# Performance work log

Hardware: AMD Instinct MI355X
Metric: run time of the kernel (lower is better)

## Reference

```python
import jax, jax.numpy as jnp
import numpy as np

# Model hyperparameters (match init_kwargs)
T = 3          # reasoning hops
L = 3          # rule channels (parallel LSTMs)
E = 50000      # number of entities
N = 1000000    # number of KG triples
R = 200        # r_size = (n-1)//2
NREL = 2 * R + 1  # n = 401 (forward rels, inverse rels, identity)
H = 256        # emb_size
TAU = 10.0     # tau_1 softmax temperature
TOPK = 1000    # top-k state pruning for hops t>=1
B = 8          # batch size


def setup_inputs() -> dict:
    key = jax.random.key(0)
    ks = jax.random.split(key, 16)
    s = 0.05
    return {
        "input_x": jax.random.randint(ks[0], (B,), 0, E),
        "input_r": jax.random.randint(ks[1], (B,), 0, NREL),
        "e2triple": jax.random.randint(ks[2], (3, N), 0, E),
        "triple2e": jax.random.randint(ks[3], (2, N), 0, E),
        "r2triple": jax.random.randint(ks[4], (1, N), 0, R),
        "emb": jax.random.normal(ks[5], (NREL, H), jnp.float32) * s,
        "Wih_f": jax.random.normal(ks[6], (L, 4 * H, H), jnp.float32) * s,
        "Whh_f": jax.random.normal(ks[7], (L, 4 * H, H), jnp.float32) * s,
        "bih_f": jax.random.normal(ks[8], (L, 4 * H), jnp.float32) * s,
        "bhh_f": jax.random.normal(ks[9], (L, 4 * H), jnp.float32) * s,
        "Wih_b": jax.random.normal(ks[10], (L, 4 * H, H), jnp.float32) * s,
        "Whh_b": jax.random.normal(ks[11], (L, 4 * H, H), jnp.float32) * s,
        "bih_b": jax.random.normal(ks[12], (L, 4 * H), jnp.float32) * s,
        "bhh_b": jax.random.normal(ks[13], (L, 4 * H), jnp.float32) * s,
        "linW": jax.random.normal(ks[14], (NREL, 2 * H), jnp.float32) * s,
        "linb": jax.random.normal(ks[15], (NREL,), jnp.float32) * s,
    }


def _lstm_scan(x, Wih, Whh, bih, bhh):
    # x: [S, B, H]; PyTorch gate order i, f, g, o. Returns hidden seq [S, B, H].
    Bn = x.shape[1]
    Hh = Whh.shape[1]
    pre = x @ Wih.T + bih + bhh  # hoist input projection out of the scan

    def step(carry, xt):
        h, c = carry
        g = xt + h @ Whh.T
        i, f, gg, o = jnp.split(g, 4, axis=-1)
        c = jax.nn.sigmoid(f) * c + jax.nn.sigmoid(i) * jnp.tanh(gg)
        h = jax.nn.sigmoid(o) * jnp.tanh(c)
        return (h, c), h

    init = (jnp.zeros((Bn, Hh), x.dtype), jnp.zeros((Bn, Hh), x.dtype))
    _, hs = jax.lax.scan(step, init, pre)
    return hs


def reference(input_x, input_r, e2triple, triple2e, r2triple, emb,
              Wih_f, Whh_f, bih_f, bhh_f, Wih_b, Whh_b, bih_b, bhh_b,
              linW, linb):
    Bsz = input_x.shape[0]
    x0 = jax.nn.one_hot(input_x, E, dtype=emb.dtype)  # [B, E] one-hot query entity
    q = emb[input_r]                                   # [B, H] query relation emb
    # [T+1, B, H]: T copies of the query rel emb, last step is the special emb[-1]
    seq = jnp.concatenate([
        jnp.broadcast_to(q[None], (T, Bsz, H)),
        jnp.broadcast_to(emb[-1][None, None, :], (1, Bsz, H)),
    ], axis=0)

    outs = []
    for l in range(L):  # small fixed number of structurally distinct LSTMs
        hf = _lstm_scan(seq, Wih_f[l], Whh_f[l], bih_f[l], bhh_f[l])
        hb = _lstm_scan(seq[::-1], Wih_b[l], Whh_b[l], bih_b[l], bhh_b[l])[::-1]
        rnn = jnp.concatenate([hf, hb], axis=-1).transpose(1, 0, 2)  # [B, T+1, 2H]
        outs.append(rnn[:, :-1] @ linW.T + linb)                      # [B, T, n]
    w_all = jnp.stack(outs, axis=2)  # [B, T, L, n]

    heads = e2triple[0]   # [N] head entity per triple
    tails = triple2e[1]   # [N] tail entity per triple
    tails2 = e2triple[2]  # [N] tail entity per triple (inverse-direction gather)
    rels = r2triple[0]    # [N] relation per triple, in [0, R)

    def propagate(x, w):
        # x: [B, *, E] entity state, w: [B, L, n] relation weights
        s_i = w[:, :, -1:] * x                              # identity relation
        msg_f = x[:, :, heads] * w[:, :, rels]              # [B, L, N] fwd messages
        s_h = jnp.zeros((Bsz, L, E), x.dtype).at[:, :, tails].add(msg_f)
        msg_b = x[:, :, tails2] * w[:, :, rels + R]         # inverse relations
        s_t = jnp.zeros((Bsz, L, E), x.dtype).at[:, :, heads].add(msg_b)
        return s_i + s_h + s_t

    def prune_topk(x, k):
        # keep top-k entity scores per (batch, channel), zero the rest
        th = jax.lax.top_k(x, k)[0][..., -1:]
        return jnp.where(x >= th, x, jnp.zeros((), x.dtype))

    s = None
    for t in range(T):
        w = jax.nn.softmax(w_all[:, t] / TAU, axis=-1)      # [B, L, n]
        xin = x0[:, None, :] if t == 0 else prune_topk(s, TOPK)
        st = propagate(xin, w)
        s = st / jnp.maximum(st.sum(-1, keepdims=True), 1e-7)
    return s.sum(axis=1)  # [B, E]
```

## Files before the change

### kernel.cpp

```cpp
#include <hip/hip_runtime.h>
#include <math.h>

#define TT 3
#define LL 3
#define EE 50000
#define NN 1000000
#define RR 200
#define NRELC 401
#define HH 256
#define BB 8
#define KTOP 1000
#define SROW 24
#define NBUCK 782
#define BSH 6
#define CSRN (2 * NN)
#define STB 512
#define SEGS 50176

__device__ __forceinline__ float sigmoidf_(float x) {
    if (x >= 0.f) { return 1.f / (1.f + expf(-x)); }
    float z = expf(x); return z / (1.f + z);
}

__global__ __launch_bounds__(256) void pre_fused(
    const int* __restrict__ input_r, const float* __restrict__ emb,
    const float* __restrict__ Wih_f, const float* __restrict__ bih_f, const float* __restrict__ bhh_f,
    const float* __restrict__ Wih_b, const float* __restrict__ bih_b, const float* __restrict__ bhh_b,
    float* __restrict__ preq, float* __restrict__ pree,
    float* __restrict__ hstate, float* __restrict__ cstate, float* __restrict__ hbuf2,
    const int* __restrict__ heads, const int* __restrict__ tails,
    unsigned* __restrict__ bh, int do_hist)
{
    if (blockIdx.x >= 384) {
        if (!do_hist) return;
        __shared__ unsigned h[NBUCK];
        int tid = threadIdx.x;
        int bid = blockIdx.x - 384;
        for (int i = tid; i < NBUCK; i += 256) h[i] = 0u;
        __syncthreads();
        for (int i = bid * 256 + tid; i < NN; i += STB * 256) {
            atomicAdd(&h[tails[i] >> BSH], 1u);
            atomicAdd(&h[heads[i] >> BSH], 1u);
        }
        __syncthreads();
        for (int j = tid; j < NBUCK; j += 256)
            bh[(size_t)j * STB + bid] = h[j];
        return;
    }
    int wave = blockIdx.x * 4 + (threadIdx.x >> 6);
    int lane = threadIdx.x & 63;
    int ld = wave >> 8;
    int j  = wave & 255;
    int l = ld >> 1, dir = ld & 1;
    const float* Wih = (dir ? Wih_b : Wih_f) + (size_t)l * 4 * HH * HH;
    const float* bih = (dir ? bih_b : bih_f) + l * 4 * HH;
    const float* bhh = (dir ? bhh_b : bhh_f) + l * 4 * HH;

    float4 xf[9];
    for (int b = 0; b < 8; ++b) {
        int r = input_r[b];
        xf[b] = *(const float4*)(emb + (size_t)r * HH + lane * 4);
    }
    xf[8] = *(const float4*)(emb + (size_t)(NRELC - 1) * HH + lane * 4);

    float g4[4], ge4[4];
    for (int q = 0; q < 4; ++q) {
        int row = q * 256 + j;
        float4 w4 = *(const float4*)(Wih + (size_t)row * HH + lane * 4);
        float acc[9];
        #pragma unroll
        for (int c = 0; c < 9; ++c)
            acc[c] = w4.x * xf[c].x + w4.y * xf[c].y + w4.z * xf[c].z + w4.w * xf[c].w;
        #pragma unroll
        for (int off = 32; off > 0; off >>= 1)
            #pragma unroll
            for (int c = 0; c < 9; ++c) acc[c] += __shfl_xor(acc[c], off);
        float bsum = bih[row] + bhh[row];
        g4[q]  = (lane < 8 ? acc[lane] : 0.f) + bsum;
        ge4[q] = acc[8] + bsum;
        if (lane < 8) preq[((size_t)ld * 8 + lane) * 1024 + row] = g4[q];
        if (lane == 8) pree[(size_t)ld * 1024 + row] = ge4[q];
    }
    if (lane < 8) {
        float gi, gg, go;
        if (dir == 0) { gi = g4[0]; gg = g4[2]; go = g4[3]; }
        else          { gi = ge4[0]; gg = ge4[2]; go = ge4[3]; }
        float c = sigmoidf_(gi) * tanhf(gg);
        float h = sigmoidf_(go) * tanhf(c);
        int g = (ld * 8 + lane) * 256 + j;
        cstate[g] = c;
        hstate[g] = h;
        if (dir == 0) hbuf2[(((size_t)ld * 8 + lane) * 3 + 0) * HH + j] = h;
    }
}

__global__ __launch_bounds__(256) void rec_fused(
    const float* __restrict__ Whh_f, const float* __restrict__ Whh_b,
    const float* __restrict__ preq, const float* __restrict__ pree,
    const float* __restrict__ hprev, float* __restrict__ hnext,
    float* __restrict__ cstate, float* __restrict__ hbuf2, int step)
{
    int wave = blockIdx.x * 4 + (threadIdx.x >> 6);
    int lane = threadIdx.x & 63;
    int ld = wave >> 8, j = wave & 255;
    int l = ld >> 1, dir = ld & 1;
    const float* Whh = (dir ? Whh_b : Whh_f) + (size_t)l * 4 * HH * HH;
    bool use_e = (dir == 0) && (step == 3);

    float4 hf[8];
    for (int b = 0; b < 8; ++b)
        hf[b] = *(const float4*)(hprev + ((size_t)ld * 8 + b) * HH + lane * 4);

    float g4[4];
    for (int q = 0; q < 4; ++q) {
        int row = q * 256 + j;
        float4 w4 = *(const float4*)(Whh + (size_t)row * HH + lane * 4);
        float acc[8];
        #pragma unroll
        for (int b = 0; b < 8; ++b)
            acc[b] = w4.x * hf[b].x + w4.y * hf[b].y + w4.z * hf[b].z + w4.w * hf[b].w;
        #pragma unroll
        for (int off = 32; off > 0; off >>= 1)
            #pragma unroll
            for (int b = 0; b < 8; ++b) acc[b] += __shfl_xor(acc[b], off);
        if (lane < 8) {
            float pre = use_e ? pree[(size_t)ld * 1024 + row]
                              : preq[((size_t)ld * 8 + lane) * 1024 + row];
            g4[q] = acc[lane] + pre;
        }
    }
    if (lane < 8) {
        int g = (ld * 8 + lane) * 256 + j;
        float c = cstate[g];
        float iv = sigmoidf_(g4[0]), fv = sigmoidf_(g4[1]);
        float gg = tanhf(g4[2]),     ov = sigmoidf_(g4[3]);
        c = fv * c + iv * gg;
        float h = ov * tanhf(c);
        cstate[g] = c;
        hnext[g] = h;
        int t_out = dir ? (3 - step) : step;
        if (t_out <= 2) hbuf2[(((size_t)ld * 8 + lane) * 3 + t_out) * HH + j] = h;
    }
}

__global__ __launch_bounds__(256) void logits_dot(
    const float* __restrict__ hbuf2, const float* __restrict__ linW,
    const float* __restrict__ linb, float* __restrict__ wbuf)
{
    int wave = blockIdx.x * 4 + (threadIdx.x >> 6);
    if (wave >= 3 * 3 * NRELC) return;
    int lane = threadIdx.x & 63;
    int n = wave % NRELC;
    int tc = wave / NRELC;
    int t = tc / 3, chunk = tc % 3;
    const float4* wr = (const float4*)(linW + (size_t)n * 2 * HH + lane * 8);
    float4 w4a = wr[0], w4b = wr[1];
    float acc[8];
    #pragma unroll
    for (int i = 0; i < 8; ++i) {
        int combo = chunk * 8 + i;
        int b = combo / 3, l = combo % 3;
        int ldh = (lane < 32) ? (l * 2 + 0) : (l * 2 + 1);
        const float* hsrc = hbuf2 + (((size_t)ldh * 8 + b) * 3 + t) * HH + (lane & 31) * 8;
        float4 f0 = *(const float4*)hsrc;
        float4 f1 = *(const float4*)(hsrc + 4);
        acc[i] = w4a.x * f0.x + w4a.y * f0.y + w4a.z * f0.z + w4a.w * f0.w
               + w4b.x * f1.x + w4b.y * f1.y + w4b.z * f1.z + w4b.w * f1.w;
    }
    #pragma unroll
    for (int off = 32; off > 0; off >>= 1)
        #pragma unroll
        for (int i = 0; i < 8; ++i) acc[i] += __shfl_xor(acc[i], off);
    if (lane < 8) {
        int combo = chunk * 8 + lane;
        wbuf[((size_t)t * 24 + combo) * NRELC + n] = acc[lane] + linb[n];
    }
}

__global__ __launch_bounds__(256) void softmax_kernel(float* __restrict__ wbuf) {
    int rowi = blockIdx.x;
    float* w = wbuf + (size_t)rowi * NRELC;
    __shared__ float red[256];
    int tid = threadIdx.x;
    float v0 = w[tid];
    float v1 = (tid + 256 < NRELC) ? w[tid + 256] : -1e30f;
    red[tid] = fmaxf(v0, v1); __syncthreads();
    for (int s2 = 128; s2 > 0; s2 >>= 1) {
        if (tid < s2) red[tid] = fmaxf(red[tid], red[tid + s2]);
        __syncthreads();
    }
    float m = red[0]; __syncthreads();
    float e0 = expf((v0 - m) * 0.1f);
    float e1 = (tid + 256 < NRELC) ? expf((v1 - m) * 0.1f) : 0.f;
    red[tid] = e0 + e1; __syncthreads();
    for (int s2 = 128; s2 > 0; s2 >>= 1) {
        if (tid < s2) red[tid] += red[tid + s2];
        __syncthreads();
    }
    float denom = red[0];
    w[tid] = e0 / denom;
    if (tid + 256 < NRELC) w[tid + 256] = e1 / denom;
}

__global__ __launch_bounds__(256) void fill_seed(
    float* __restrict__ s, const int* __restrict__ input_x, const float* __restrict__ w0,
    unsigned* __restrict__ rowcnt)
{
    __shared__ int xs[8];
    __shared__ float wv[24];
    if (threadIdx.x < 8) xs[threadIdx.x] = input_x[threadIdx.x];
    if (threadIdx.x < 24) wv[threadIdx.x] = w0[(size_t)threadIdx.x * NRELC + (NRELC - 1)];
    if (blockIdx.x == 0 && threadIdx.x < 24) rowcnt[threadIdx.x] = 0u;
    __syncthreads();
    int i = blockIdx.x * 256 + threadIdx.x;
    if (i >= SROW * EE) return;
    int row = i % 24;
    int e = i / 24;
    s[i] = (e == xs[row / 3]) ? wv[row] : 0.f;
}

__global__ __launch_bounds__(256) void hop0_scan(
    const int* __restrict__ heads, const int* __restrict__ tails,
    const int* __restrict__ tails2, const int* __restrict__ rels,
    const int* __restrict__ input_x, const float* __restrict__ w0,
    float* __restrict__ s)
{
    __shared__ int xs[BB];
    if (threadIdx.x < BB) xs[threadIdx.x] = input_x[threadIdx.x];
    __syncthreads();
    int i = blockIdx.x * 256 + threadIdx.x;
    if (i >= NN) return;
    int h = heads[i], t2 = tails2[i];
    bool any = false;
    #pragma unroll
    for (int b = 0; b < BB; ++b) any = any || (h == xs[b]) || (t2 == xs[b]);
    if (!any) return;
    int tl = tails[i], rr = rels[i];
    for (int b = 0; b < BB; ++b) {
        if (h == xs[b])
            for (int l = 0; l < LL; ++l)
                atomicAdd(&s[(size_t)tl * SROW + b * 3 + l], w0[(b * 3 + l) * NRELC + rr]);
        if (t2 == xs[b])
            for (int l = 0; l < LL; ++l)
                atomicAdd(&s[(size_t)h * SROW + b * 3 + l], w0[(b * 3 + l) * NRELC + rr + RR]);
    }
}

__global__ __launch_bounds__(256) void rowsum_compact(
    const float* __restrict__ s, float* __restrict__ partial,
    unsigned* __restrict__ ckey, unsigned* __restrict__ rowcnt, int do_compact)
{
    __shared__ float acc[24];
    __shared__ unsigned lkey[24][168];
    __shared__ unsigned lcnt[24];
    __shared__ unsigned lbase[24];
    int tid = threadIdx.x;
    if (tid < 24) { acc[tid] = 0.f; lcnt[tid] = 0u; }
    __syncthreads();
    int gidx = blockIdx.x * 256 + tid;
    int row = gidx % 24;
    float a = 0.f;
    const int total = SROW * EE;
    for (int k = 0; k < 13; ++k) {
        long i = (long)gidx + (long)k * 98304;
        if (i < total) {
            float v = s[i];
            a += v;
            if (do_compact && __float_as_uint(v) != 0u) {
                unsigned slot = atomicAdd(&lcnt[row], 1u);
                slot = min(slot, 167u);
                lkey[row][slot] = __float_as_uint(v);
            }
        }
    }
    if (do_compact) {
        __syncthreads();
        if (tid < 24) {
            unsigned c = min(lcnt[tid], 168u);
            lcnt[tid] = c;
            lbase[tid] = min(atomicAdd(&rowcnt[tid], c), (unsigned)SEGS);
        }
        __syncthreads();
        int r = tid % 24;
        int nthr = (r < 16) ? 11 : 10;
        unsigned cnt = lcnt[r], base = lbase[r];
        if (base + cnt > (unsigned)SEGS) cnt = (unsigned)SEGS - base;
        for (unsigned j = (unsigned)(tid / 24); j < cnt; j += nthr)
            ckey[(size_t)r * SEGS + base + j] = lkey[r][j];
        __syncthreads();
    }
    atomicAdd(&acc[row], a);
    __syncthreads();
    if (tid < 24) partial[blockIdx.x * 24 + tid] = acc[tid];
}

__global__ __launch_bounds__(256) void rowsum_fin(
    const float* __restrict__ partial, float* __restrict__ sums,
    const float* __restrict__ w_t, float* __restrict__ wsc,
    float* __restrict__ wTg)
{
    int r = blockIdx.x;
    int tid = threadIdx.x;
    __shared__ float sa;
    if (tid == 0) {
        float a = 0.f;
        for (int j = 0; j < 384; ++j) a += partial[j * 24 + r];
        a = fmaxf(a, 1e-7f);
        sums[r] = a;
        sa = a;
    }
    __syncthreads();
    if (w_t != nullptr) {
        float a = sa;
        for (int i = tid; i < NRELC; i += 256) {
            float v = w_t[(size_t)r * NRELC + i] / a;
            wsc[(size_t)r * NRELC + i] = v;
            if (wTg != nullptr && i < 2 * RR) wTg[(size_t)i * SROW + r] = v;
        }
    }
}

__global__ __launch_bounds__(256) void rowsum_fin2(
    const float* __restrict__ partial2, float* __restrict__ sums,
    const float* __restrict__ w_t, float* __restrict__ wsc,
    float* __restrict__ wTg)
{
    int r = blockIdx.x;
    int tid = threadIdx.x;
    __shared__ float red[256];
    float a = 0.f;
    for (int g = tid; g < NBUCK; g += 256) a += partial2[(size_t)g * 24 + r];
    red[tid] = a; __syncthreads();
    for (int s2 = 128; s2 > 0; s2 >>= 1) {
        if (tid < s2) red[tid] += red[tid + s2];
        __syncthreads();
    }
    __shared__ float sa;
    if (tid == 0) { sa = fmaxf(red[0], 1e-7f); sums[r] = sa; }
    __syncthreads();
    if (w_t != nullptr) {
        float aa = sa;
        for (int i = tid; i < NRELC; i += 256) {
            float v = w_t[(size_t)r * NRELC + i] / aa;
            wsc[(size_t)r * NRELC + i] = v;
            if (wTg != nullptr && i < 2 * RR) wTg[(size_t)i * SROW + r] = v;
        }
    }
}

__global__ __launch_bounds__(512) void topk_select(
    const unsigned* __restrict__ ckey, const unsigned* __restrict__ rowcnt,
    float* __restrict__ th, int* __restrict__ mask)
{
    int row = blockIdx.x, tid = threadIdx.x;
    {
        int per = (EE + 23) / 24;
        int e0 = row * per, e1 = min(e0 + per, EE);
        for (int e = e0 + tid; e < e1; e += 512) mask[e] = 0;
    }
    const unsigned* keys = ckey + (size_t)row * SEGS;
    int n = min((int)rowcnt[row], SEGS);
    __shared__ unsigned hist[256];
    __shared__ int red[256];
    __shared__ int sh_bin, sh_rem;
    unsigned prefix = 0;
    int remk = KTOP;
    int iters = (n + 511) / 512;
    int lane = tid & 63;
    for (int round = 0; round < 4; ++round) {
        if (tid < 256) hist[tid] = 0u;
        __syncthreads();
        int shift = 24 - 8 * round;
        for (int it = 0; it < iters; ++it) {
            int i = it * 512 + tid;
            bool valid = (i < n);
            unsigned key = valid ? keys[i] : 0u;
            valid = valid && (round == 0 || (key >> (shift + 8)) == prefix);
            unsigned bin = valid ? ((key >> shift) & 255u) : 0u;
            unsigned long long peers = __ballot(valid);
            #pragma unroll
            for (int bit = 0; bit < 8; ++bit) {
                unsigned long long bm = __ballot(valid && ((bin >> bit) & 1u));
                peers &= ((bin >> bit) & 1u) ? bm : ~bm;
            }
            if (valid) {
                unsigned long long lower = peers & ((1ull << lane) - 1ull);
                if (lower == 0ull)
                    atomicAdd(&hist[bin], (unsigned)__popcll(peers));
            }
        }
        __syncthreads();
        if (tid < 256) red[tid] = (int)hist[tid];
        __syncthreads();
        for (int off = 1; off < 256; off <<= 1) {
            int v = 0;
            if (tid < 256 && tid + off < 256) v = red[tid + off];
            __syncthreads();
            if (tid < 256) red[tid] += v;
            __syncthreads();
        }
        if (tid == 0) { sh_bin = 0; sh_rem = remk; }
        __syncthreads();
        if (tid < 256) {
            int cnt = (int)hist[tid];
            int above = (tid == 255) ? 0 : red[tid + 1];
            if (above < remk && above + cnt >= remk) { sh_bin = tid; sh_rem = remk - above; }
        }
        __syncthreads();
        prefix = (prefix << 8) | (unsigned)sh_bin;
        remk = sh_rem;
        __syncthreads();
    }
    if (tid == 0) th[row] = __uint_as_float(prefix);
}

__global__ __launch_bounds__(256) void prune_flat(
    float* __restrict__ s, const float* __restrict__ th,
    const float* __restrict__ wsc, float* __restrict__ x, int* __restrict__ mask,
    unsigned* __restrict__ rowcnt, int write_s)
{
    __shared__ float ths[24], w4s[24];
    if (threadIdx.x < 24) {
        ths[threadIdx.x] = th[threadIdx.x];
        w4s[threadIdx.x] = wsc[threadIdx.x * NRELC + (NRELC - 1)];
    }
    if (blockIdx.x == 0 && threadIdx.x < 24) rowcnt[threadIdx.x] = 0u;
    __syncthreads();
    int i = blockIdx.x * 256 + threadIdx.x;
    if (i >= SROW * EE) return;
    int row = i % 24;
    int e = i / 24;
    float v = s[i];
    float xv = (v >= ths[row]) ? v : 0.f;
    x[i] = xv;
    if (write_s) s[i] = w4s[row] * xv;
    if (xv > 0.f) atomicOr(&mask[e], 1 << (row / 3));
}

__global__ __launch_bounds__(256) void hop_scan(
    const int* __restrict__ heads, const int* __restrict__ tails,
    const int* __restrict__ tails2, const int* __restrict__ rels,
    const int* __restrict__ mask, const float* __restrict__ x,
    const float* __restrict__ wsc, float* __restrict__ s)
{
    int gid = blockIdx.x * 256 + threadIdx.x;
    int i = gid >> 3;
    if (i >= NN) return;
    int b = gid & 7;
    int h = heads[i], t2 = tails2[i];
    int mh = mask[h], mt = mask[t2];
    bool ah = (mh >> b) & 1;
    bool at = (mt >> b) & 1;
    if (!(ah || at)) return;
    int tl = tails[i], rr = rels[i];
    int row = b * 3;
    if (ah) {
        float v0 = x[(size_t)h * SROW + row];
        float v1 = x[(size_t)h * SROW + row + 1];
        float v2 = x[(size_t)h * SROW + row + 2];
        if (v0 != 0.f) atomicAdd(&s[(size_t)tl * SROW + row],     v0 * wsc[(row)     * NRELC + rr]);
        if (v1 != 0.f) atomicAdd(&s[(size_t)tl * SROW + row + 1], v1 * wsc[(row + 1) * NRELC + rr]);
        if (v2 != 0.f) atomicAdd(&s[(size_t)tl * SROW + row + 2], v2 * wsc[(row + 2) * NRELC + rr]);
    }
    if (at) {
        float v0 = x[(size_t)t2 * SROW + row];
        float v1 = x[(size_t)t2 * SROW + row + 1];
        float v2 = x[(size_t)t2 * SROW + row + 2];
        if (v0 != 0.f) atomicAdd(&s[(size_t)h * SROW + row],     v0 * wsc[(row)     * NRELC + rr + RR]);
        if (v1 != 0.f) atomicAdd(&s[(size_t)h * SROW + row + 1], v1 * wsc[(row + 1) * NRELC + rr + RR]);
        if (v2 != 0.f) atomicAdd(&s[(size_t)h * SROW + row + 2], v2 * wsc[(row + 2) * NRELC + rr + RR]);
    }
}

__global__ __launch_bounds__(512) void csr_scanb(
    unsigned* __restrict__ bh, unsigned* __restrict__ gcnt)
{
    __shared__ unsigned sc[STB];
    int bk = blockIdx.x, tid = threadIdx.x;
    unsigned v = bh[(size_t)bk * STB + tid];
    sc[tid] = v; __syncthreads();
    #pragma unroll
    for (int o = 1; o < STB; o <<= 1) {
        unsigned u = (tid >= o) ? sc[tid - o] : 0u;
        __syncthreads();
        sc[tid] += u;
        __syncthreads();
    }
    bh[(size_t)bk * STB + tid] = sc[tid] - v;
    if (tid == STB - 1) gcnt[bk] = sc[tid];
}

__global__ __launch_bounds__(1024) void csr_scan2(
    const unsigned* __restrict__ gcnt, unsigned* __restrict__ gOff)
{
    __shared__ unsigned sc[1024];
    int tid = threadIdx.x;
    unsigned v = (tid < NBUCK) ? gcnt[tid] : 0u;
    sc[tid] = v; __syncthreads();
    #pragma unroll
    for (int o = 1; o < 1024; o <<= 1) {
        unsigned u = (tid >= o) ? sc[tid - o] : 0u;
        __syncthreads();
        sc[tid] += u;
        __syncthreads();
    }
    if (tid < NBUCK) gOff[tid] = sc[tid] - v;
    if (tid == NBUCK - 1) gOff[NBUCK] = sc[tid];
}

__global__ __launch_bounds__(256) void csr_stage2(
    const int* __restrict__ heads, const int* __restrict__ tails,
    const int* __restrict__ tails2, const int* __restrict__ rels,
    const unsigned* __restrict__ gOff, const unsigned* __restrict__ bh,
    unsigned* __restrict__ staging)
{
    __shared__ unsigned base[NBUCK];
    __shared__ unsigned cur[NBUCK];
    int tid = threadIdx.x;
    for (int j = tid; j < NBUCK; j += 256) {
        base[j] = gOff[j] + bh[(size_t)j * STB + blockIdx.x];
        cur[j] = 0u;
    }
    __syncthreads();
    for (int i = blockIdx.x * 256 + tid; i < NN; i += STB * 256) {
        unsigned rl = (unsigned)rels[i];
        int h = heads[i], d1 = tails[i], t2 = tails2[i];
        unsigned p1 = base[d1 >> BSH] + atomicAdd(&cur[d1 >> BSH], 1u);
        if (p1 < (unsigned)CSRN)
            staging[p1] = ((unsigned)(d1 & 63) << 26) | ((unsigned)h << 9) | rl;
        unsigned p2 = base[h >> BSH] + atomicAdd(&cur[h >> BSH], 1u);
        if (p2 < (unsigned)CSRN)
            staging[p2] = ((unsigned)(h & 63) << 26) | ((unsigned)t2 << 9) | (rl + RR);
    }
}

__global__ __launch_bounds__(256) void hop_bucket(
    const unsigned* __restrict__ gOff, const unsigned* __restrict__ staging,
    const int* __restrict__ mask, const float* __restrict__ x,
    const float* __restrict__ wT, const float* __restrict__ wsc,
    float* __restrict__ s, float* __restrict__ partial2,
    unsigned* __restrict__ ckey, unsigned* __restrict__ rowcnt, int do_compact)
{
    __shared__ float sl[64][24];
    __shared__ float w4s[24];
    __shared__ float acc24[24];
    __shared__ unsigned lcnt[24];
    __shared__ unsigned lbase[24];
    __shared__ unsigned lkey[24][64];
    int bk = blockIdx.x, tid = threadIdx.x;
    for (int i = tid; i < 64 * 24; i += 256) ((float*)sl)[i] = 0.f;
    if (tid < 24) {
        w4s[tid] = wsc[tid * NRELC + (NRELC - 1)];
        acc24[tid] = 0.f;
        lcnt[tid] = 0u;
    }
    __syncthreads();
    unsigned j0 = gOff[bk], j1 = gOff[bk + 1];
    for (unsigned j = j0 + tid; j < j1; j += 256) {
        unsigned p = staging[j];
        int src = (int)((p >> 9) & 0xFFFFu);
        int m = mask[src];
        if (!m) continue;
        int dl = (int)(p >> 26);
        int rel = (int)(p & 511u);
        const float* xs = x + (size_t)src * SROW;
        const float* wr = wT + (size_t)rel * SROW;
        while (m) {
            int b = __ffs(m) - 1; m &= m - 1;
            int r = b * 3;
            atomicAdd(&sl[dl][r],     xs[r]     * wr[r]);
            atomicAdd(&sl[dl][r + 1], xs[r + 1] * wr[r + 1]);
            atomicAdd(&sl[dl][r + 2], xs[r + 2] * wr[r + 2]);
        }
    }
    __syncthreads();
    int e0 = bk * 64;
    for (int idx = tid; idx < 64 * 24; idx += 256) {
        int el = idx / 24, row = idx % 24;
        int e = e0 + el;
        if (e >= EE) continue;
        float v = sl[el][row] + w4s[row] * x[(size_t)e * SROW + row];
        s[(size_t)e * SROW + row] = v;
        atomicAdd(&acc24[row], v);
        if (do_compact && __float_as_uint(v) != 0u) {
            unsigned slot = atomicAdd(&lcnt[row], 1u);
            slot = min(slot, 63u);
            lkey[row][slot] = __float_as_uint(v);
        }
    }
    __syncthreads();
    if (tid < 24) partial2[(size_t)bk * 24 + tid] = acc24[tid];
    if (do_compact) {
        if (tid < 24) {
            unsigned c = min(lcnt[tid], 64u);
            lcnt[tid] = c;
            lbase[tid] = min(atomicAdd(&rowcnt[tid], c), (unsigned)SEGS);
        }
        __syncthreads();
        int r = tid % 24;
        int nthr = (r < 16) ? 11 : 10;
        unsigned cnt = lcnt[r], base = lbase[r];
        if (base + cnt > (unsigned)SEGS) cnt = (unsigned)SEGS - base;
        for (unsigned j = (unsigned)(tid / 24); j < cnt; j += nthr)
            ckey[(size_t)r * SEGS + base + j] = lkey[r][j];
    }
}

__global__ void final_kernel(const float* __restrict__ s, const float* __restrict__ sums,
                             float* __restrict__ out) {
    __shared__ float ss[24];
    if (threadIdx.x < 24) ss[threadIdx.x] = sums[threadIdx.x];
    __syncthreads();
    int e = blockIdx.x * 256 + threadIdx.x;
    if (e >= EE) return;
    const float* se = s + (size_t)e * SROW;
    #pragma unroll
    for (int b = 0; b < 8; ++b)
        out[(size_t)b * EE + e] = se[b * 3] / ss[b * 3]
                                + se[b * 3 + 1] / ss[b * 3 + 1]
                                + se[b * 3 + 2] / ss[b * 3 + 2];
}

extern "C" void kernel_launch(void* const* d_in, const int* in_sizes, int n_in,
                              void* d_out, int out_size, void* d_ws, size_t ws_size,
                              hipStream_t stream)
{
    const int*   input_x  = (const int*)d_in[0];
    const int*   input_r  = (const int*)d_in[1];
    const int*   e2triple = (const int*)d_in[2];
    const int*   triple2e = (const int*)d_in[3];
    const int*   r2triple = (const int*)d_in[4];
    const float* emb      = (const float*)d_in[5];
    const float* Wih_f    = (const float*)d_in[6];
    const float* Whh_f    = (const float*)d_in[7];
    const float* bih_f    = (const float*)d_in[8];
    const float* bhh_f    = (const float*)d_in[9];
    const float* Wih_b    = (const float*)d_in[10];
    const float* Whh_b    = (const float*)d_in[11];
    const float* bih_b    = (const float*)d_in[12];
    const float* bhh_b    = (const float*)d_in[13];
    const float* linW     = (const float*)d_in[14];
    const float* linb     = (const float*)d_in[15];

    const int* heads  = e2triple;
    const int* tails2 = e2triple + 2 * (size_t)NN;
    const int* tails  = triple2e + (size_t)NN;
    const int* rels   = r2triple;

    float* ws      = (float*)d_ws;
    float* hbuf    = ws;
    float* wbuf    = hbuf + 36864;
    float* xst     = wbuf + 28872;
    float* sst     = xst + 1200000;
    float* sums    = sst + 1200000;
    float* th      = sums + 24;
    int*   mask    = (int*)(th + 24);
    float* partial = (float*)(mask + EE);
    unsigned* rowcnt  = (unsigned*)(partial + 9216);
    float* partial2   = (float*)(rowcnt + 32);
    unsigned* ckey    = (unsigned*)(partial2 + NBUCK * 24);
    unsigned* bh      = ckey + 24 * (size_t)SEGS;
    unsigned* gcnt    = bh + (size_t)NBUCK * STB;
    unsigned* gOff    = gcnt + 784;
    unsigned* staging = gOff + 800;
    float*    wT      = (float*)(staging + CSRN);
    const size_t NEED = (size_t)((wT + 9600) - ws) * 4;
    const bool use_csr = (ws_size >= NEED);
    float* wsc     = hbuf;
    float* preq    = xst;
    float* pree    = preq + 49152;
    float* hstateA = pree + 6144;
    float* hstateB = hstateA + 12288;
    float* cstate  = hstateB + 12288;

    float* out = (float*)d_out;
    const int EBLK  = (EE + 255) / 256;
    const int SBLK  = (SROW * EE + 255) / 256;
    const int NBLK  = (NN + 255) / 256;
    const int N8BLK = (NN * 8) / 256;

    pre_fused<<<896, 256, 0, stream>>>(input_r, emb, Wih_f, bih_f, bhh_f,
                                       Wih_b, bih_b, bhh_b, preq, pree,
                                       hstateA, cstate, hbuf,
                                       heads, tails, bh, use_csr ? 1 : 0);
    rec_fused<<<384, 256, 0, stream>>>(Whh_f, Whh_b, preq, pree, hstateA, hstateB,
                                       cstate, hbuf, 1);
    rec_fused<<<384, 256, 0, stream>>>(Whh_f, Whh_b, preq, pree, hstateB, hstateA,
                                       cstate, hbuf, 2);
    rec_fused<<<384, 256, 0, stream>>>(Whh_f, Whh_b, preq, pree, hstateA, hstateB,
                                       cstate, hbuf, 3);
    logits_dot<<<903, 256, 0, stream>>>(hbuf, linW, linb, wbuf);
    softmax_kernel<<<72, 256, 0, stream>>>(wbuf);

    if (use_csr) {
        csr_scanb<<<NBUCK, 512, 0, stream>>>(bh, gcnt);
        csr_scan2<<<1, 1024, 0, stream>>>(gcnt, gOff);
        csr_stage2<<<STB, 256, 0, stream>>>(heads, tails, tails2, rels, gOff, bh, staging);
    }

    fill_seed<<<SBLK, 256, 0, stream>>>(sst, input_x, wbuf, rowcnt);
    hop0_scan<<<NBLK, 256, 0, stream>>>(heads, tails, tails2, rels, input_x, wbuf, sst);
    rowsum_compact<<<384, 256, 0, stream>>>(sst, partial, ckey, rowcnt, 1);
    rowsum_fin<<<24, 256, 0, stream>>>(partial, sums, wbuf + 1 * 24 * NRELC, wsc,
                                       use_csr ? wT : nullptr);

    for (int t = 1; t < TT; ++t) {
        topk_select<<<24, 512, 0, stream>>>(ckey, rowcnt, th, mask);
        prune_flat<<<SBLK, 256, 0, stream>>>(sst, th, wsc, xst, mask, rowcnt,
                                             use_csr ? 0 : 1);
        const float* w_next = (t + 1 < TT) ? (wbuf + (size_t)(t + 1) * 24 * NRELC) : nullptr;
        if (use_csr) {
            hop_bucket<<<NBUCK, 256, 0, stream>>>(gOff, staging, mask, xst, wT, wsc,
                                                  sst, partial2, ckey, rowcnt,
                                                  (t + 1 < TT) ? 1 : 0);
            rowsum_fin2<<<24, 256, 0, stream>>>(partial2, sums, w_next, wsc, wT);
        } else {
            hop_scan<<<N8BLK, 256, 0, stream>>>(heads, tails, tails2, rels, mask, xst, wsc, sst);
            rowsum_compact<<<384, 256, 0, stream>>>(sst, partial, ckey, rowcnt,
                                                    (t + 1 < TT) ? 1 : 0);
            rowsum_fin<<<24, 256, 0, stream>>>(partial, sums, w_next, wsc, nullptr);
        }
    }

    final_kernel<<<EBLK, 256, 0, stream>>>(sst, sums, out);
}
```

Before: 316.3 us.

## Route hop 0 through CSR bucket kernel and fuse top-k pruning into hop

On the CSR path, the first hop now builds a seed-entity mask and runs the bucketed gather kernel with a transposed softmax weight table, replacing the seed fill, full triple scan and separate row-sum compaction. For later hops, the materialised pruned state buffer is dropped: a mask-build kernel marks surviving entities, and the hop kernel applies the top-k threshold while reading the previous state. This removes several full passes over the entity state and the triple list, at the cost of extra threshold comparisons and atomicOr traffic when building the mask.

```diff
diff --git a/kernel.cpp b/kernel.cpp
--- a/kernel.cpp
+++ b/kernel.cpp
@@ -177,7 +177,9 @@
     }
 }
 
-__global__ __launch_bounds__(256) void softmax_kernel(float* __restrict__ wbuf) {
+__global__ __launch_bounds__(256) void softmax_kernel(
+    float* __restrict__ wbuf, float* __restrict__ wT0)
+{
     int rowi = blockIdx.x;
     float* w = wbuf + (size_t)rowi * NRELC;
     __shared__ float red[256];
@@ -198,8 +200,45 @@
         __syncthreads();
     }
     float denom = red[0];
-    w[tid] = e0 / denom;
-    if (tid + 256 < NRELC) w[tid + 256] = e1 / denom;
+    float o0 = e0 / denom;
+    w[tid] = o0;
+    float o1 = 0.f;
+    if (tid + 256 < NRELC) { o1 = e1 / denom; w[tid + 256] = o1; }
+    if (wT0 != nullptr && rowi < 24) {
+        if (tid < 2 * RR) wT0[(size_t)tid * SROW + rowi] = o0;
+        if (tid + 256 < 2 * RR) wT0[(size_t)(tid + 256) * SROW + rowi] = o1;
+    }
+}
+
+__global__ __launch_bounds__(256) void mask0_build(
+    int* __restrict__ mask, const int* __restrict__ input_x,
+    unsigned* __restrict__ rowcnt)
+{
+    __shared__ int xs[8];
+    if (threadIdx.x < 8) xs[threadIdx.x] = input_x[threadIdx.x];
+    if (blockIdx.x == 0 && threadIdx.x < 24) rowcnt[threadIdx.x] = 0u;
+    __syncthreads();
+    int e = blockIdx.x * 256 + threadIdx.x;
+    if (e >= EE) return;
+    int m = 0;
+    #pragma unroll
+    for (int b = 0; b < 8; ++b) if (e == xs[b]) m |= 1 << b;
+    mask[e] = m;
+}
+
+__global__ __launch_bounds__(256) void mask_build(
+    const float* __restrict__ s, const float* __restrict__ th,
+    int* __restrict__ mask, unsigned* __restrict__ rowcnt)
+{
+    __shared__ float ths[24];
+    if (threadIdx.x < 24) ths[threadIdx.x] = th[threadIdx.x];
+    if (blockIdx.x == 0 && threadIdx.x < 24) rowcnt[threadIdx.x] = 0u;
+    __syncthreads();
+    int i = blockIdx.x * 256 + threadIdx.x;
+    if (i >= SROW * EE) return;
+    int row = i % 24;
+    float v = s[i];
+    if (v >= ths[row]) atomicOr(&mask[i / 24], 1 << (row / 3));
 }
 
 __global__ __launch_bounds__(256) void fill_seed(
@@ -536,13 +575,17 @@
 
 __global__ __launch_bounds__(256) void hop_bucket(
     const unsigned* __restrict__ gOff, const unsigned* __restrict__ staging,
-    const int* __restrict__ mask, const float* __restrict__ x,
+    const int* __restrict__ mask, const float* __restrict__ sprev,
+    const float* __restrict__ th, const int* __restrict__ input_x,
     const float* __restrict__ wT, const float* __restrict__ wsc,
-    float* __restrict__ s, float* __restrict__ partial2,
-    unsigned* __restrict__ ckey, unsigned* __restrict__ rowcnt, int do_compact)
+    float* __restrict__ snext, float* __restrict__ partial2,
+    unsigned* __restrict__ ckey, unsigned* __restrict__ rowcnt,
+    int do_compact, int is_t0)
 {
     __shared__ float sl[64][24];
     __shared__ float w4s[24];
+    __shared__ float ths[24];
+    __shared__ int   xs8[8];
     __shared__ float acc24[24];
     __shared__ unsigned lcnt[24];
     __shared__ unsigned lbase[24];
@@ -551,9 +594,11 @@
     for (int i = tid; i < 64 * 24; i += 256) ((float*)sl)[i] = 0.f;
     if (tid < 24) {
         w4s[tid] = wsc[tid * NRELC + (NRELC - 1)];
+        ths[tid] = is_t0 ? 0.f : th[tid];
         acc24[tid] = 0.f;
         lcnt[tid] = 0u;
     }
+    if (tid < 8) xs8[tid] = is_t0 ? input_x[tid] : 0;
     __syncthreads();
     unsigned j0 = gOff[bk], j1 = gOff[bk + 1];
     for (unsigned j = j0 + tid; j < j1; j += 256) {
@@ -563,14 +608,27 @@
         if (!m) continue;
         int dl = (int)(p >> 26);
         int rel = (int)(p & 511u);
-        const float* xs = x + (size_t)src * SROW;
         const float* wr = wT + (size_t)rel * SROW;
-        while (m) {
-            int b = __ffs(m) - 1; m &= m - 1;
-            int r = b * 3;
-            atomicAdd(&sl[dl][r],     xs[r]     * wr[r]);
-            atomicAdd(&sl[dl][r + 1], xs[r + 1] * wr[r + 1]);
-            atomicAdd(&sl[dl][r + 2], xs[r + 2] * wr[r + 2]);
+        if (is_t0) {
+            while (m) {
+                int b = __ffs(m) - 1; m &= m - 1;
+                int r = b * 3;
+                atomicAdd(&sl[dl][r],     wr[r]);
+                atomicAdd(&sl[dl][r + 1], wr[r + 1]);
+                atomicAdd(&sl[dl][r + 2], wr[r + 2]);
+            }
+        } else {
+            const float* xsrow = sprev + (size_t)src * SROW;
+            while (m) {
+                int b = __ffs(m) - 1; m &= m - 1;
+                int r = b * 3;
+                float x0 = xsrow[r];     x0 = (x0 >= ths[r])     ? x0 : 0.f;
+                float x1 = xsrow[r + 1]; x1 = (x1 >= ths[r + 1]) ? x1 : 0.f;
+                float x2 = xsrow[r + 2]; x2 = (x2 >= ths[r + 2]) ? x2 : 0.f;
+                atomicAdd(&sl[dl][r],     x0 * wr[r]);
+                atomicAdd(&sl[dl][r + 1], x1 * wr[r + 1]);
+                atomicAdd(&sl[dl][r + 2], x2 * wr[r + 2]);
+            }
         }
     }
     __syncthreads();
@@ -579,8 +637,15 @@
         int el = idx / 24, row = idx % 24;
         int e = e0 + el;
         if (e >= EE) continue;
-        float v = sl[el][row] + w4s[row] * x[(size_t)e * SROW + row];
-        s[(size_t)e * SROW + row] = v;
+        float xv;
+        if (is_t0) {
+            xv = (e == xs8[row / 3]) ? 1.f : 0.f;
+        } else {
+            float u = sprev[(size_t)e * SROW + row];
+            xv = (u >= ths[row]) ? u : 0.f;
+        }
+        float v = sl[el][row] + w4s[row] * xv;
+        snext[(size_t)e * SROW + row] = v;
         atomicAdd(&acc24[row], v);
         if (do_compact && __float_as_uint(v) != 0u) {
             unsigned slot = atomicAdd(&lcnt[row], 1u);
@@ -650,9 +715,9 @@
     float* ws      = (float*)d_ws;
     float* hbuf    = ws;
     float* wbuf    = hbuf + 36864;
-    float* xst     = wbuf + 28872;
-    float* sst     = xst + 1200000;
-    float* sums    = sst + 1200000;
+    float* sstA    = wbuf + 28872;
+    float* sstB    = sstA + 1200000;
+    float* sums    = sstB + 1200000;
     float* th      = sums + 24;
     int*   mask    = (int*)(th + 24);
     float* partial = (float*)(mask + EE);
@@ -664,10 +729,11 @@
     unsigned* gOff    = gcnt + 784;
     unsigned* staging = gOff + 800;
     float*    wT      = (float*)(staging + CSRN);
-    const size_t NEED = (size_t)((wT + 9600) - ws) * 4;
+    float*    wT0     = wT + 9600;
+    const size_t NEED = (size_t)((wT0 + 9600) - ws) * 4;
     const bool use_csr = (ws_size >= NEED);
     float* wsc     = hbuf;
-    float* preq    = xst;
+    float* preq    = sstA;
     float* pree    = preq + 49152;
     float* hstateA = pree + 6144;
     float* hstateB = hstateA + 12288;
@@ -690,7 +756,7 @@
     rec_fused<<<384, 256, 0, stream>>>(Whh_f, Whh_b, preq, pree, hstateA, hstateB,
                                        cstate, hbuf, 3);
     logits_dot<<<903, 256, 0, stream>>>(hbuf, linW, linb, wbuf);
-    softmax_kernel<<<72, 256, 0, stream>>>(wbuf);
+    softmax_kernel<<<72, 256, 0, stream>>>(wbuf, use_csr ? wT0 : nullptr);
 
     if (use_csr) {
         csr_scanb<<<NBUCK, 512, 0, stream>>>(bh, gcnt);
@@ -698,29 +764,41 @@
         csr_stage2<<<STB, 256, 0, stream>>>(heads, tails, tails2, rels, gOff, bh, staging);
     }
 
-    fill_seed<<<SBLK, 256, 0, stream>>>(sst, input_x, wbuf, rowcnt);
-    hop0_scan<<<NBLK, 256, 0, stream>>>(heads, tails, tails2, rels, input_x, wbuf, sst);
-    rowsum_compact<<<384, 256, 0, stream>>>(sst, partial, ckey, rowcnt, 1);
-    rowsum_fin<<<24, 256, 0, stream>>>(partial, sums, wbuf + 1 * 24 * NRELC, wsc,
-                                       use_csr ? wT : nullptr);
-
-    for (int t = 1; t < TT; ++t) {
+    if (use_csr) {
+        mask0_build<<<EBLK, 256, 0, stream>>>(mask, input_x, rowcnt);
+        hop_bucket<<<NBUCK, 256, 0, stream>>>(gOff, staging, mask, nullptr, nullptr,
+                                              input_x, wT0, wbuf, sstA, partial2,
+                                              ckey, rowcnt, 1, 1);
+        rowsum_fin2<<<24, 256, 0, stream>>>(partial2, sums, wbuf + 1 * 24 * NRELC, wsc, wT);
         topk_select<<<24, 512, 0, stream>>>(ckey, rowcnt, th, mask);
-        prune_flat<<<SBLK, 256, 0, stream>>>(sst, th, wsc, xst, mask, rowcnt,
-                                             use_csr ? 0 : 1);
-        const float* w_next = (t + 1 < TT) ? (wbuf + (size_t)(t + 1) * 24 * NRELC) : nullptr;
-        if (use_csr) {
-            hop_bucket<<<NBUCK, 256, 0, stream>>>(gOff, staging, mask, xst, wT, wsc,
-                                                  sst, partial2, ckey, rowcnt,
-                                                  (t + 1 < TT) ? 1 : 0);
-            rowsum_fin2<<<24, 256, 0, stream>>>(partial2, sums, w_next, wsc, wT);
-        } else {
+        mask_build<<<SBLK, 256, 0, stream>>>(sstA, th, mask, rowcnt);
+        hop_bucket<<<NBUCK, 256, 0, stream>>>(gOff, staging, mask, sstA, th,
+                                              input_x, wT, wsc, sstB, partial2,
+                                              ckey, rowcnt, 1, 0);
+        rowsum_fin2<<<24, 256, 0, stream>>>(partial2, sums, wbuf + 2 * 24 * NRELC, wsc, wT);
+        topk_select<<<24, 512, 0, stream>>>(ckey, rowcnt, th, mask);
+        mask_build<<<SBLK, 256, 0, stream>>>(sstB, th, mask, rowcnt);
+        hop_bucket<<<NBUCK, 256, 0, stream>>>(gOff, staging, mask, sstB, th,
+                                              input_x, wT, wsc, sstA, partial2,
+                                              ckey, rowcnt, 0, 0);
+        rowsum_fin2<<<24, 256, 0, stream>>>(partial2, sums, nullptr, nullptr, nullptr);
+        final_kernel<<<EBLK, 256, 0, stream>>>(sstA, sums, out);
+    } else {
+        float* xst = sstA;
+        float* sst = sstB;
+        fill_seed<<<SBLK, 256, 0, stream>>>(sst, input_x, wbuf, rowcnt);
+        hop0_scan<<<NBLK, 256, 0, stream>>>(heads, tails, tails2, rels, input_x, wbuf, sst);
+        rowsum_compact<<<384, 256, 0, stream>>>(sst, partial, ckey, rowcnt, 1);
+        rowsum_fin<<<24, 256, 0, stream>>>(partial, sums, wbuf + 1 * 24 * NRELC, wsc, nullptr);
+        for (int t = 1; t < TT; ++t) {
+            topk_select<<<24, 512, 0, stream>>>(ckey, rowcnt, th, mask);
+            prune_flat<<<SBLK, 256, 0, stream>>>(sst, th, wsc, xst, mask, rowcnt, 1);
             hop_scan<<<N8BLK, 256, 0, stream>>>(heads, tails, tails2, rels, mask, xst, wsc, sst);
             rowsum_compact<<<384, 256, 0, stream>>>(sst, partial, ckey, rowcnt,
                                                     (t + 1 < TT) ? 1 : 0);
+            const float* w_next = (t + 1 < TT) ? (wbuf + (size_t)(t + 1) * 24 * NRELC) : nullptr;
             rowsum_fin<<<24, 256, 0, stream>>>(partial, sums, w_next, wsc, nullptr);
         }
-    }
-
-    final_kernel<<<EBLK, 256, 0, stream>>>(sst, sums, out);
-}
+        final_kernel<<<EBLK, 256, 0, stream>>>(sst, sums, out);
+    }
+}
```

Result: slower. 675.9 us (+113.7%).
